# Kernel tuning notes

Hardware: AMD Instinct MI355X
Metric: run time of the kernel (lower is better)

The kernel has to match this reference:

```python
import jax, jax.numpy as jnp
import numpy as np

E_PHI = 1024
E_F = 1024
HID = 1024
N_HEADS = 16
HEAD_DIM = HID // N_HEADS


def setup_inputs() -> dict:
    key = jax.random.key(0)
    ks = jax.random.split(key, 9)
    B, S = 2, 2048
    s = 0.02
    return {
        "q": jax.random.normal(ks[0], (B, S, E_PHI), jnp.float32),
        "k": jax.random.normal(ks[1], (B, S, E_PHI), jnp.float32),
        "v": jax.random.normal(ks[2], (B, S, E_F), jnp.float32),
        "W_q": jax.random.normal(ks[3], (E_PHI, HID), jnp.float32) * s,
        "W_k": jax.random.normal(ks[4], (E_PHI, HID), jnp.float32) * s,
        "W_v": jax.random.normal(ks[5], (E_F, HID), jnp.float32) * s,
        "b_v": jax.random.normal(ks[6], (HID,), jnp.float32) * s,
        "W_o": jax.random.normal(ks[7], (HID, E_F), jnp.float32) * s,
        "b_o": jax.random.normal(ks[8], (E_F,), jnp.float32) * s,
    }


def reference(q, k, v, W_q, W_k, W_v, b_v, W_o, b_o):
    B, S, _ = q.shape
    # projections -> [B, S, n_heads, head_dim]
    qh = (q @ W_q).reshape(B, S, N_HEADS, HEAD_DIM)
    kh = (k @ W_k).reshape(B, S, N_HEADS, HEAD_DIM)
    vh = (v @ W_v + b_v).reshape(B, S, N_HEADS, HEAD_DIM)

    scale = 1.0 / jnp.sqrt(jnp.float32(HEAD_DIM))
    # scores: [B, H, S_q, S_k]
    scores = jnp.einsum("bihd,bjhd->bhij", qh, kh) * scale

    i = jnp.arange(S)[:, None]
    j = jnp.arange(S)[None, :]
    # strict causal (j < i) plus the single (0,0) entry
    keep = (j < i) | ((i == 0) & (j == 0))
    scores = jnp.where(keep, scores, jnp.float32(-jnp.inf))

    probs = jax.nn.softmax(scores, axis=-1)
    attn = jnp.einsum("bhij,bjhd->bihd", probs, vh).reshape(B, S, HID)
    # dropout is identity in eval mode
    return attn @ W_o + b_o
```

## Files before the change

kernel.cpp:

```cpp
#include <hip/hip_runtime.h>
#include <hip/hip_bf16.h>

typedef __attribute__((ext_vector_type(8))) short bf16x8;
typedef __attribute__((ext_vector_type(4))) float f32x4;

typedef __attribute__((address_space(1))) const void gv_t;
typedef __attribute__((address_space(3))) void lv_t;

static __device__ __forceinline__ void gload16(const void* g, void* l) {
    __builtin_amdgcn_global_load_lds((gv_t*)g, (lv_t*)l, 16, 0, 0);
}

static __device__ __forceinline__ f32x4 mfma16(bf16x8 a, bf16x8 b, f32x4 c) {
    return __builtin_amdgcn_mfma_f32_16x16x32_bf16(a, b, c, 0, 0, 0);
}

static __device__ __forceinline__ unsigned short f2bf(float x) {
    unsigned u = __builtin_bit_cast(unsigned, x);
    u = u + 0x7FFFu + ((u >> 16) & 1u);
    return (unsigned short)(u >> 16);
}

#define NN 1024
#define KK 1024
#define BK 32
#define NKT (KK / BK)
#define AP 72
#define SOFF2 17.3123404907f

__global__ void cvt3_k(const float* __restrict__ q, const float* __restrict__ k,
                       const float* __restrict__ v, unsigned short* __restrict__ dst)
{
    const int z = blockIdx.y;
    const float* src = (z == 0) ? q : (z == 1) ? k : v;
    unsigned short* d = dst + (size_t)z * 4194304u;
    const size_t i = ((size_t)blockIdx.x * 256 + threadIdx.x) * 8;
    float4 a = *reinterpret_cast<const float4*>(&src[i]);
    float4 b = *reinterpret_cast<const float4*>(&src[i + 4]);
    bf16x8 o;
    o[0] = (short)f2bf(a.x); o[1] = (short)f2bf(a.y);
    o[2] = (short)f2bf(a.z); o[3] = (short)f2bf(a.w);
    o[4] = (short)f2bf(b.x); o[5] = (short)f2bf(b.y);
    o[6] = (short)f2bf(b.z); o[7] = (short)f2bf(b.w);
    *reinterpret_cast<bf16x8*>(&d[i]) = o;
}

__global__ void trcvt_k(const float* __restrict__ w0, const float* __restrict__ w1,
                        const float* __restrict__ w2, const float* __restrict__ w3,
                        unsigned short* __restrict__ dst)
{
    const int z = blockIdx.z;
    const float* W = (z == 0) ? w0 : (z == 1) ? w1 : (z == 2) ? w2 : w3;
    unsigned short* D = dst + (size_t)z * 1048576u;
    __shared__ float t[32][33];
    const int tx = threadIdx.x, ty = threadIdx.y;
    const int x  = blockIdx.x * 32 + tx;
    const int y0 = blockIdx.y * 32;
    for (int i = ty; i < 32; i += 8) t[i][tx] = W[(size_t)(y0 + i) * 1024 + x];
    __syncthreads();
    const int xo = y0 + tx;
    for (int i = ty; i < 32; i += 8)
        D[(size_t)(blockIdx.x * 32 + i) * 1024 + xo] = f2bf(t[tx][i]);
}

__global__ void vtr_k(const unsigned short* __restrict__ vh, unsigned short* __restrict__ vt)
{
    __shared__ unsigned short t[32][33];
    const int bh = blockIdx.z;
    const int b = bh >> 4, h = bh & 15;
    const int s0 = blockIdx.x * 32;
    const int d0 = blockIdx.y * 32;
    const int tx = threadIdx.x, ty = threadIdx.y;
    for (int i = ty; i < 32; i += 8)
        t[i][tx] = vh[(size_t)(b * 2048 + s0 + i) * 1024 + h * 64 + d0 + tx];
    __syncthreads();
    for (int i = ty; i < 32; i += 8)
        vt[((size_t)bh * 64 + d0 + i) * 2048 + s0 + tx] = t[tx][i];
}

template<int MODE>
__global__ __launch_bounds__(256, 2)
void gemm2_k(const unsigned short* __restrict__ Abase,
             const unsigned short* __restrict__ Btbase,
             void* __restrict__ Cbase,
             const float* __restrict__ bias)
{
    __shared__ unsigned short As[2][4096];
    __shared__ unsigned short Bs[2][4096];

    const int z = blockIdx.z;
    const unsigned short* A  = Abase  + (size_t)z * 4194304u;
    const unsigned short* Bt = Btbase + (size_t)z * 1048576u;

    const int tid = threadIdx.x;
    const int wid = tid >> 6, lane = tid & 63;
    const int lg = lane >> 4, lc = lane & 15;
    const int brow = blockIdx.x * 128;
    const int bcol = blockIdx.y * 128;
    const int wr = (wid >> 1) * 64;
    const int wc = (wid & 1) * 64;

    const int srow = tid >> 2;
    const int scol = (tid & 3) * 8;

    f32x4 acc[4][4];
#pragma unroll
    for (int i = 0; i < 4; ++i)
#pragma unroll
        for (int j = 0; j < 4; ++j) acc[i][j] = (f32x4){0.f, 0.f, 0.f, 0.f};

    gload16(&A [(size_t)(brow + srow)      * KK + scol], &As[0][tid * 8]);
    gload16(&A [(size_t)(brow + 64 + srow) * KK + scol], &As[0][2048 + tid * 8]);
    gload16(&Bt[(size_t)(bcol + srow)      * KK + scol], &Bs[0][tid * 8]);
    gload16(&Bt[(size_t)(bcol + 64 + srow) * KK + scol], &Bs[0][2048 + tid * 8]);
    __syncthreads();

    int cur = 0;
    for (int kt = 0; kt < NKT; ++kt) {
        if (kt + 1 < NKT) {
            const int k0 = (kt + 1) * BK;
            gload16(&A [(size_t)(brow + srow)      * KK + k0 + scol], &As[cur ^ 1][tid * 8]);
            gload16(&A [(size_t)(brow + 64 + srow) * KK + k0 + scol], &As[cur ^ 1][2048 + tid * 8]);
            gload16(&Bt[(size_t)(bcol + srow)      * KK + k0 + scol], &Bs[cur ^ 1][tid * 8]);
            gload16(&Bt[(size_t)(bcol + 64 + srow) * KK + k0 + scol], &Bs[cur ^ 1][2048 + tid * 8]);
        }
        bf16x8 af[4], bfr[4];
#pragma unroll
        for (int i = 0; i < 4; ++i)
            af[i] = *reinterpret_cast<const bf16x8*>(&As[cur][(wr + i * 16 + lc) * 32 + lg * 8]);
#pragma unroll
        for (int j = 0; j < 4; ++j)
            bfr[j] = *reinterpret_cast<const bf16x8*>(&Bs[cur][(wc + j * 16 + lc) * 32 + lg * 8]);
#pragma unroll
        for (int i = 0; i < 4; ++i)
#pragma unroll
            for (int j = 0; j < 4; ++j)
                acc[i][j] = mfma16(af[i], bfr[j], acc[i][j]);
        __syncthreads();
        cur ^= 1;
    }

    float scale = 1.0f;
    const float* bp = nullptr;
    if (MODE == 0) { if (z == 0) scale = 0.18033688f; if (z == 2) bp = bias; }
    else           { bp = bias; }

#pragma unroll
    for (int j = 0; j < 4; ++j) {
        const int col = bcol + wc + j * 16 + lc;
        const float bb = bp ? bp[col] : 0.0f;
#pragma unroll
        for (int i = 0; i < 4; ++i) {
            const int row0 = brow + wr + i * 16 + lg * 4;
#pragma unroll
            for (int r = 0; r < 4; ++r) {
                const float val = acc[i][j][r] * scale + bb;
                if (MODE == 0)
                    ((unsigned short*)Cbase)[(size_t)z * 4194304u + (size_t)(row0 + r) * NN + col] = f2bf(val);
                else
                    ((float*)Cbase)[(size_t)(row0 + r) * NN + col] = val;
            }
        }
    }
}

__global__ __launch_bounds__(256, 4)
void attn_k(const unsigned short* __restrict__ qh,
            const unsigned short* __restrict__ kh,
            const unsigned short* __restrict__ vt,
            unsigned short* __restrict__ out)
{
    __shared__ unsigned short Ks[64 * AP];
    __shared__ unsigned short Vs[64 * AP];
    __shared__ unsigned short Pl[4][16 * AP];

    const int id = blockIdx.x;
    const int u  = id >> 5;
    const int qt = (u < 16) ? u : 47 - u;
    const int bh = (id & 7) * 4 + ((id >> 3) & 3);
    const int b = bh >> 4, h = bh & 15;
    const int tid = threadIdx.x, wid = tid >> 6, lane = tid & 63;
    const int lg = lane >> 4, lc = lane & 15;
    const int q0w = qt * 64 + wid * 16;

    const size_t base = (size_t)b * 2048u * 1024u + (size_t)h * 64u;
    const unsigned short* Qb  = qh + base;
    const unsigned short* Kb  = kh + base;
    const unsigned short* Vtb = vt + (size_t)bh * 131072u;

    const int r0 = tid >> 3, kof = (tid & 7) * 8;

    bf16x8 qf[2];
#pragma unroll
    for (int s = 0; s < 2; ++s)
        qf[s] = *reinterpret_cast<const bf16x8*>(&Qb[(size_t)(q0w + lc) * 1024 + s * 32 + lg * 8]);

    f32x4 acc_o[4];
#pragma unroll
    for (int d = 0; d < 4; ++d) acc_o[d] = (f32x4){0.f, 0.f, 0.f, 0.f};
    float lrow[4] = {0.f, 0.f, 0.f, 0.f};

    bf16x8 ka0 = *reinterpret_cast<const bf16x8*>(&Kb [(size_t)(r0)      * 1024 + kof]);
    bf16x8 ka1 = *reinterpret_cast<const bf16x8*>(&Kb [(size_t)(32 + r0) * 1024 + kof]);
    bf16x8 va0 = *reinterpret_cast<const bf16x8*>(&Vtb[(size_t)(r0)      * 2048 + kof]);
    bf16x8 va1 = *reinterpret_cast<const bf16x8*>(&Vtb[(size_t)(32 + r0) * 2048 + kof]);

    for (int kt = 0; kt <= qt; ++kt) {
        const int k0 = kt * 64;
        __syncthreads();
        *reinterpret_cast<bf16x8*>(&Ks[(r0)      * AP + kof]) = ka0;
        *reinterpret_cast<bf16x8*>(&Ks[(32 + r0) * AP + kof]) = ka1;
        *reinterpret_cast<bf16x8*>(&Vs[(r0)      * AP + kof]) = va0;
        *reinterpret_cast<bf16x8*>(&Vs[(32 + r0) * AP + kof]) = va1;
        __syncthreads();

        if (kt < qt) {
            const int kn = k0 + 64;
            ka0 = *reinterpret_cast<const bf16x8*>(&Kb [(size_t)(kn + r0)      * 1024 + kof]);
            ka1 = *reinterpret_cast<const bf16x8*>(&Kb [(size_t)(kn + 32 + r0) * 1024 + kof]);
            va0 = *reinterpret_cast<const bf16x8*>(&Vtb[(size_t)(r0)      * 2048 + kn + kof]);
            va1 = *reinterpret_cast<const bf16x8*>(&Vtb[(size_t)(32 + r0) * 2048 + kn + kof]);
        }

        f32x4 sc[4];
#pragma unroll
        for (int g = 0; g < 4; ++g) sc[g] = (f32x4){0.f, 0.f, 0.f, 0.f};
#pragma unroll
        for (int s = 0; s < 2; ++s)
#pragma unroll
            for (int g = 0; g < 4; ++g) {
                bf16x8 kf = *reinterpret_cast<const bf16x8*>(
                    &Ks[(g * 16 + lc) * AP + s * 32 + lg * 8]);
                sc[g] = mfma16(qf[s], kf, sc[g]);
            }

        if (kt == qt) {
#pragma unroll
            for (int g = 0; g < 4; ++g)
#pragma unroll
                for (int r = 0; r < 4; ++r) {
                    const int qi = q0w + lg * 4 + r;
                    const int ki = k0 + g * 16 + lc;
                    const bool keep = (ki < qi) || (qi == 0 && ki == 0);
                    if (!keep) sc[g][r] = -1e30f;
                }
        }

#pragma unroll
        for (int r = 0; r < 4; ++r) {
            float p0 = exp2f(sc[0][r] - SOFF2);
            float p1 = exp2f(sc[1][r] - SOFF2);
            float p2 = exp2f(sc[2][r] - SOFF2);
            float p3 = exp2f(sc[3][r] - SOFF2);
            lrow[r] += (p0 + p1) + (p2 + p3);
            const int prow = (lg * 4 + r) * AP;
            Pl[wid][prow + 0 * 16 + lc] = f2bf(p0);
            Pl[wid][prow + 1 * 16 + lc] = f2bf(p1);
            Pl[wid][prow + 2 * 16 + lc] = f2bf(p2);
            Pl[wid][prow + 3 * 16 + lc] = f2bf(p3);
        }
        __builtin_amdgcn_sched_barrier(0);

#pragma unroll
        for (int s = 0; s < 2; ++s) {
            bf16x8 pfr = *reinterpret_cast<const bf16x8*>(
                &Pl[wid][lc * AP + s * 32 + lg * 8]);
#pragma unroll
            for (int d = 0; d < 4; ++d) {
                bf16x8 vf = *reinterpret_cast<const bf16x8*>(
                    &Vs[(d * 16 + lc) * AP + s * 32 + lg * 8]);
                acc_o[d] = mfma16(pfr, vf, acc_o[d]);
            }
        }
        __builtin_amdgcn_sched_barrier(0);
    }

#pragma unroll
    for (int r = 0; r < 4; ++r) {
        float s0 = lrow[r];
        s0 += __shfl_xor(s0, 1); s0 += __shfl_xor(s0, 2);
        s0 += __shfl_xor(s0, 4); s0 += __shfl_xor(s0, 8);
        lrow[r] = s0;
    }

#pragma unroll
    for (int r = 0; r < 4; ++r) {
        const float inv = 1.0f / lrow[r];
        const size_t orow = (size_t)(b * 2048 + q0w + lg * 4 + r) * 1024 + (size_t)h * 64;
#pragma unroll
        for (int d = 0; d < 4; ++d)
            out[orow + d * 16 + lc] = f2bf(acc_o[d][r] * inv);
    }
}

extern "C" void kernel_launch(void* const* d_in, const int* in_sizes, int n_in,
                              void* d_out, int out_size, void* d_ws, size_t ws_size,
                              hipStream_t stream)
{
    const float* q   = (const float*)d_in[0];
    const float* k   = (const float*)d_in[1];
    const float* v   = (const float*)d_in[2];
    const float* W_q = (const float*)d_in[3];
    const float* W_k = (const float*)d_in[4];
    const float* W_v = (const float*)d_in[5];
    const float* b_v = (const float*)d_in[6];
    const float* W_o = (const float*)d_in[7];
    const float* b_o = (const float*)d_in[8];

    char* w = (char*)d_ws;
    unsigned short* qkvb = (unsigned short*)w;
    unsigned short* Wt   = (unsigned short*)(w + 25165824);
    unsigned short* ph   = (unsigned short*)(w + 33554432);
    unsigned short* attn = (unsigned short*)(w + 58720256);
    unsigned short* vt   = qkvb;

    cvt3_k <<<dim3(2048, 3, 1), 256, 0, stream>>>(q, k, v, qkvb);
    trcvt_k<<<dim3(32, 32, 4), dim3(32, 8, 1), 0, stream>>>(W_q, W_k, W_v, W_o, Wt);
    gemm2_k<0><<<dim3(32, 8, 3), 256, 0, stream>>>(qkvb, Wt, ph, b_v);
    vtr_k  <<<dim3(64, 2, 32), dim3(32, 8, 1), 0, stream>>>(ph + 2 * 4194304, vt);
    attn_k <<<dim3(1024, 1, 1), 256, 0, stream>>>(ph, ph + 4194304, vt, attn);
    gemm2_k<1><<<dim3(32, 8, 1), 256, 0, stream>>>(attn, Wt + 3 * 1048576, d_out, b_o);
}
```

Measured before the change: 131.7 us.

## Keep attention probabilities in registers via transposed MFMA and remap GEMM blocks per XCD

The attention kernel now computes the transposed score tile (K as the A operand), so each lane holds probabilities for a single query column. The probabilities are packed to bf16 and rearranged with cross-lane shuffles into the B operand of the PV MFMA, which removes the per-wave LDS staging buffer and its write/read round trip. Output stores become packed 8-byte writes, and the row-sum reduction needs fewer shuffles. Separately, the GEMM grid is flattened to 1D and remapped so adjacent row tiles land on the same XCD for L2 reuse, and f2bf now uses the compiler's native bf16 conversion.

```diff
diff --git a/kernel.cpp b/kernel.cpp
--- a/kernel.cpp
+++ b/kernel.cpp
@@ -3,6 +3,7 @@
 
 typedef __attribute__((ext_vector_type(8))) short bf16x8;
 typedef __attribute__((ext_vector_type(4))) float f32x4;
+typedef __attribute__((ext_vector_type(4))) unsigned u32x4;
 
 typedef __attribute__((address_space(1))) const void gv_t;
 typedef __attribute__((address_space(3))) void lv_t;
@@ -16,9 +17,11 @@
 }
 
 static __device__ __forceinline__ unsigned short f2bf(float x) {
-    unsigned u = __builtin_bit_cast(unsigned, x);
-    u = u + 0x7FFFu + ((u >> 16) & 1u);
-    return (unsigned short)(u >> 16);
+    __bf16 b = (__bf16)x;
+    return __builtin_bit_cast(unsigned short, b);
+}
+static __device__ __forceinline__ unsigned pk2(float lo, float hi) {
+    return (unsigned)f2bf(lo) | ((unsigned)f2bf(hi) << 16);
 }
 
 #define NN 1024
@@ -88,15 +91,22 @@
     __shared__ unsigned short As[2][4096];
     __shared__ unsigned short Bs[2][4096];
 
-    const int z = blockIdx.z;
+    const int f   = blockIdx.x;
+    const int xcd = f & 7;
+    const int g   = f >> 3;
+    const int z   = g >> 5;
+    const int rr  = g & 31;
+    const int bx  = xcd * 4 + (rr & 3);
+    const int by  = rr >> 2;
+
     const unsigned short* A  = Abase  + (size_t)z * 4194304u;
     const unsigned short* Bt = Btbase + (size_t)z * 1048576u;
 
     const int tid = threadIdx.x;
     const int wid = tid >> 6, lane = tid & 63;
     const int lg = lane >> 4, lc = lane & 15;
-    const int brow = blockIdx.x * 128;
-    const int bcol = blockIdx.y * 128;
+    const int brow = bx * 128;
+    const int bcol = by * 128;
     const int wr = (wid >> 1) * 64;
     const int wc = (wid & 1) * 64;
 
@@ -172,7 +182,6 @@
 {
     __shared__ unsigned short Ks[64 * AP];
     __shared__ unsigned short Vs[64 * AP];
-    __shared__ unsigned short Pl[4][16 * AP];
 
     const int id = blockIdx.x;
     const int u  = id >> 5;
@@ -182,6 +191,9 @@
     const int tid = threadIdx.x, wid = tid >> 6, lane = tid & 63;
     const int lg = lane >> 4, lc = lane & 15;
     const int q0w = qt * 64 + wid * 16;
+    const int hi = lg >> 1;
+    const int srcA = ((lg & 1) << 5) | lc;
+    const int srcB = srcA + 16;
 
     const size_t base = (size_t)b * 2048u * 1024u + (size_t)h * 64u;
     const unsigned short* Qb  = qh + base;
@@ -195,10 +207,10 @@
     for (int s = 0; s < 2; ++s)
         qf[s] = *reinterpret_cast<const bf16x8*>(&Qb[(size_t)(q0w + lc) * 1024 + s * 32 + lg * 8]);
 
-    f32x4 acc_o[4];
-#pragma unroll
-    for (int d = 0; d < 4; ++d) acc_o[d] = (f32x4){0.f, 0.f, 0.f, 0.f};
-    float lrow[4] = {0.f, 0.f, 0.f, 0.f};
+    f32x4 accT[4];
+#pragma unroll
+    for (int d = 0; d < 4; ++d) accT[d] = (f32x4){0.f, 0.f, 0.f, 0.f};
+    float lsum = 0.f;
 
     bf16x8 ka0 = *reinterpret_cast<const bf16x8*>(&Kb [(size_t)(r0)      * 1024 + kof]);
     bf16x8 ka1 = *reinterpret_cast<const bf16x8*>(&Kb [(size_t)(32 + r0) * 1024 + kof]);
@@ -231,65 +243,73 @@
             for (int g = 0; g < 4; ++g) {
                 bf16x8 kf = *reinterpret_cast<const bf16x8*>(
                     &Ks[(g * 16 + lc) * AP + s * 32 + lg * 8]);
-                sc[g] = mfma16(qf[s], kf, sc[g]);
+                sc[g] = mfma16(kf, qf[s], sc[g]);
             }
 
         if (kt == qt) {
+            const int qi = q0w + lc;
 #pragma unroll
             for (int g = 0; g < 4; ++g)
 #pragma unroll
                 for (int r = 0; r < 4; ++r) {
-                    const int qi = q0w + lg * 4 + r;
-                    const int ki = k0 + g * 16 + lc;
+                    const int ki = k0 + g * 16 + lg * 4 + r;
                     const bool keep = (ki < qi) || (qi == 0 && ki == 0);
                     if (!keep) sc[g][r] = -1e30f;
                 }
         }
 
-#pragma unroll
-        for (int r = 0; r < 4; ++r) {
-            float p0 = exp2f(sc[0][r] - SOFF2);
-            float p1 = exp2f(sc[1][r] - SOFF2);
-            float p2 = exp2f(sc[2][r] - SOFF2);
-            float p3 = exp2f(sc[3][r] - SOFF2);
-            lrow[r] += (p0 + p1) + (p2 + p3);
-            const int prow = (lg * 4 + r) * AP;
-            Pl[wid][prow + 0 * 16 + lc] = f2bf(p0);
-            Pl[wid][prow + 1 * 16 + lc] = f2bf(p1);
-            Pl[wid][prow + 2 * 16 + lc] = f2bf(p2);
-            Pl[wid][prow + 3 * 16 + lc] = f2bf(p3);
-        }
-        __builtin_amdgcn_sched_barrier(0);
+        float p[4][4];
+#pragma unroll
+        for (int g = 0; g < 4; ++g)
+#pragma unroll
+            for (int r = 0; r < 4; ++r) {
+                p[g][r] = exp2f(sc[g][r] - SOFF2);
+                lsum += p[g][r];
+            }
+
+        unsigned w[4][2];
+#pragma unroll
+        for (int g = 0; g < 4; ++g) {
+            w[g][0] = pk2(p[g][0], p[g][1]);
+            w[g][1] = pk2(p[g][2], p[g][3]);
+        }
 
 #pragma unroll
         for (int s = 0; s < 2; ++s) {
-            bf16x8 pfr = *reinterpret_cast<const bf16x8*>(
-                &Pl[wid][lc * AP + s * 32 + lg * 8]);
-#pragma unroll
-            for (int d = 0; d < 4; ++d) {
+            unsigned a0A = __shfl(w[2 * s][0],     srcA);
+            unsigned a1A = __shfl(w[2 * s][1],     srcA);
+            unsigned b0A = __shfl(w[2 * s][0],     srcB);
+            unsigned b1A = __shfl(w[2 * s][1],     srcB);
+            unsigned a0B = __shfl(w[2 * s + 1][0], srcA);
+            unsigned a1B = __shfl(w[2 * s + 1][1], srcA);
+            unsigned b0B = __shfl(w[2 * s + 1][0], srcB);
+            unsigned b1B = __shfl(w[2 * s + 1][1], srcB);
+            u32x4 fr;
+            fr[0] = hi ? a0B : a0A;
+            fr[1] = hi ? a1B : a1A;
+            fr[2] = hi ? b0B : b0A;
+            fr[3] = hi ? b1B : b1A;
+            bf16x8 pb = __builtin_bit_cast(bf16x8, fr);
+#pragma unroll
+            for (int di = 0; di < 4; ++di) {
                 bf16x8 vf = *reinterpret_cast<const bf16x8*>(
-                    &Vs[(d * 16 + lc) * AP + s * 32 + lg * 8]);
-                acc_o[d] = mfma16(pfr, vf, acc_o[d]);
+                    &Vs[(di * 16 + lc) * AP + s * 32 + lg * 8]);
+                accT[di] = mfma16(vf, pb, accT[di]);
             }
         }
-        __builtin_amdgcn_sched_barrier(0);
     }
 
-#pragma unroll
-    for (int r = 0; r < 4; ++r) {
-        float s0 = lrow[r];
-        s0 += __shfl_xor(s0, 1); s0 += __shfl_xor(s0, 2);
-        s0 += __shfl_xor(s0, 4); s0 += __shfl_xor(s0, 8);
-        lrow[r] = s0;
-    }
-
-#pragma unroll
-    for (int r = 0; r < 4; ++r) {
-        const float inv = 1.0f / lrow[r];
-        const size_t orow = (size_t)(b * 2048 + q0w + lg * 4 + r) * 1024 + (size_t)h * 64;
-#pragma unroll
-        for (int d = 0; d < 4; ++d)
-            out[orow + d * 16 + lc] = f2bf(acc_o[d][r] * inv);
+    lsum += __shfl_xor(lsum, 16);
+    lsum += __shfl_xor(lsum, 32);
+    const float inv = 1.0f / lsum;
+
+    const size_t orow = (size_t)(b * 2048 + q0w + lc) * 1024 + (size_t)h * 64 + lg * 4;
+#pragma unroll
+    for (int di = 0; di < 4; ++di) {
+        unsigned lo  = pk2(accT[di][0] * inv, accT[di][1] * inv);
+        unsigned hi2 = pk2(accT[di][2] * inv, accT[di][3] * inv);
+        uint2 st; st.x = lo; st.y = hi2;
+        *reinterpret_cast<uint2*>(&out[orow + di * 16]) = st;
     }
 }
 
@@ -316,8 +336,8 @@
 
     cvt3_k <<<dim3(2048, 3, 1), 256, 0, stream>>>(q, k, v, qkvb);
     trcvt_k<<<dim3(32, 32, 4), dim3(32, 8, 1), 0, stream>>>(W_q, W_k, W_v, W_o, Wt);
-    gemm2_k<0><<<dim3(32, 8, 3), 256, 0, stream>>>(qkvb, Wt, ph, b_v);
+    gemm2_k<0><<<dim3(768, 1, 1), 256, 0, stream>>>(qkvb, Wt, ph, b_v);
     vtr_k  <<<dim3(64, 2, 32), dim3(32, 8, 1), 0, stream>>>(ph + 2 * 4194304, vt);
     attn_k <<<dim3(1024, 1, 1), 256, 0, stream>>>(ph, ph + 4194304, vt, attn);
-    gemm2_k<1><<<dim3(32, 8, 1), 256, 0, stream>>>(attn, Wt + 3 * 1048576, d_out, b_o);
-}
+    gemm2_k<1><<<dim3(256, 1, 1), 256, 0, stream>>>(attn, Wt + 3 * 1048576, d_out, b_o);
+}
```

After: 133.7 us. No clear change (+1.5%).
